# Optimization experiments

Measured on AMD Instinct MI355X. Metric: run time of the kernel, lower is better.

Reference implementation:

```python
import jax, jax.numpy as jnp
import numpy as np

N_NODES = 100000
N_EDGES = 1600000
IN_DIM = 128
OUT_DIM = 64


def setup_inputs() -> dict:
    key = jax.random.key(0)
    k1, k2, k3 = jax.random.split(key, 3)
    x = jax.random.normal(k1, (N_NODES, IN_DIM), dtype=jnp.float32)
    edge_index = jax.random.randint(k2, (2, N_EDGES), 0, N_NODES, dtype=jnp.int64)
    W = jax.random.normal(k3, (IN_DIM, OUT_DIM), dtype=jnp.float32) * (1.0 / np.sqrt(IN_DIM))
    b = jnp.zeros((OUT_DIM,), dtype=jnp.float32)
    return {"x": x, "edge_index": edge_index, "W": W, "b": b}


def reference(x, edge_index, W, b):
    row = edge_index[0]  # source nodes
    col = edge_index[1]  # target nodes (aggregation index)
    n = x.shape[0]

    # gcn_norm with add_self_loops=False: degree from edge weights (ones) at target
    ones = jnp.ones((edge_index.shape[1],), dtype=x.dtype)
    deg = jax.ops.segment_sum(ones, col, num_segments=n)  # [N]
    deg_inv_sqrt = jnp.where(deg > 0, jax.lax.rsqrt(jnp.maximum(deg, 1e-12)), 0.0)
    norm = deg_inv_sqrt[row] * deg_inv_sqrt[col]  # [E]

    # linear transform first (bias added after aggregation, as in PyG GCNConv)
    h = x @ W  # [N, OUT_DIM]

    # gather source features, scale by norm, scatter-add to targets
    msg = h[row] * norm[:, None]  # [E, OUT_DIM]
    out = jax.ops.segment_sum(msg, col, num_segments=n) + b  # [N, OUT_DIM]

    return jax.nn.relu(out)
```

## Files before the change

kernel.cpp:

```cpp
#include <hip/hip_runtime.h>
#include <hip/hip_bf16.h>

#define IN_DIM 128
#define OUT_DIM 64
#define NPB_LOG 9
#define NPB (1 << NPB_LOG)
#define MAXBUCK 1024
#define B1 1024
#define SCAN_TPB 256

static inline size_t align_up(size_t v, size_t a) { return (v + a - 1) & ~(a - 1); }

__device__ __forceinline__ float bf2f(unsigned short u) {
    return __uint_as_float(((unsigned int)u) << 16);
}
__device__ __forceinline__ unsigned short f2bf(float f) {
    unsigned int x = __float_as_uint(f);
    unsigned int r = (x + 0x7fffu + ((x >> 16) & 1u)) >> 16;
    return (unsigned short)r;
}

typedef _Float16 half8 __attribute__((ext_vector_type(8)));
typedef float f32x4 __attribute__((ext_vector_type(4)));

__global__ void __launch_bounds__(256) kA_count(
    const int* __restrict__ col, int* __restrict__ Hist,
    int n_edges, int nbuck, int chunk) {
    __shared__ int hist[MAXBUCK];
    for (int i = threadIdx.x; i < nbuck; i += 256) hist[i] = 0;
    __syncthreads();
    int start = blockIdx.x * chunk;
    int end = min(n_edges, start + chunk);
    for (int i = start + threadIdx.x; i < end; i += 256)
        atomicAdd(&hist[col[i] >> NPB_LOG], 1);
    __syncthreads();
    int* hrow = Hist + (size_t)blockIdx.x * nbuck;
    for (int i = threadIdx.x; i < nbuck; i += 256) hrow[i] = hist[i];
}

__global__ void __launch_bounds__(256) kS1_scanbins(
    const int* __restrict__ Hist, int* __restrict__ Offs,
    int* __restrict__ BinTotal, int nbuck) {
    __shared__ int s[SCAN_TPB];
    int bin = blockIdx.x;
    int t = threadIdx.x;
    int v[4];
#pragma unroll
    for (int j = 0; j < 4; ++j) v[j] = Hist[(size_t)(t * 4 + j) * nbuck + bin];
    int tsum = v[0] + v[1] + v[2] + v[3];
    s[t] = tsum;
    __syncthreads();
    for (int off = 1; off < SCAN_TPB; off <<= 1) {
        int x = (t >= off) ? s[t - off] : 0;
        __syncthreads();
        s[t] += x;
        __syncthreads();
    }
    int run = s[t] - tsum;
#pragma unroll
    for (int j = 0; j < 4; ++j) {
        Offs[(size_t)(t * 4 + j) * nbuck + bin] = run;
        run += v[j];
    }
    if (t == SCAN_TPB - 1) BinTotal[bin] = run;
}

__global__ void __launch_bounds__(256) kS2_scantotals(
    const int* __restrict__ BinTotal, int* __restrict__ BucketStart,
    int* __restrict__ row_start, int nbuck, int n_nodes, int n_edges) {
    __shared__ int s[SCAN_TPB];
    int t = threadIdx.x;
    int v[4];
#pragma unroll
    for (int j = 0; j < 4; ++j) {
        int idx = t * 4 + j;
        v[j] = (idx < nbuck) ? BinTotal[idx] : 0;
    }
    int tsum = v[0] + v[1] + v[2] + v[3];
    s[t] = tsum;
    __syncthreads();
    for (int off = 1; off < SCAN_TPB; off <<= 1) {
        int x = (t >= off) ? s[t - off] : 0;
        __syncthreads();
        s[t] += x;
        __syncthreads();
    }
    int run = s[t] - tsum;
#pragma unroll
    for (int j = 0; j < 4; ++j) {
        int idx = t * 4 + j;
        if (idx < nbuck) BucketStart[idx] = run;
        run += v[j];
    }
    if (t == 0) {
        BucketStart[nbuck] = n_edges;
        row_start[n_nodes] = n_edges;
    }
}

__global__ void __launch_bounds__(256) kB_scatter(
    const int* __restrict__ row, const int* __restrict__ col,
    const int* __restrict__ BucketStart, const int* __restrict__ Offs,
    unsigned int* __restrict__ EdgeBuf, int n_edges, int nbuck, int chunk) {
    __shared__ int cur[MAXBUCK];
    const int* orow = Offs + (size_t)blockIdx.x * nbuck;
    for (int i = threadIdx.x; i < nbuck; i += 256)
        cur[i] = BucketStart[i] + orow[i];
    __syncthreads();
    int start = blockIdx.x * chunk;
    int end = min(n_edges, start + chunk);
    for (int i = start + threadIdx.x; i < end; i += 256) {
        int c = col[i];
        int r = row[i];
        int bin = c >> NPB_LOG;
        int p = atomicAdd(&cur[bin], 1);
        EdgeBuf[p] = ((unsigned int)r << NPB_LOG) | (unsigned int)(c & (NPB - 1));
    }
}

__global__ void __launch_bounds__(256) kC_localsort(
    const unsigned int* __restrict__ EdgeBuf, const int* __restrict__ BucketStart,
    int* __restrict__ row_start, float* __restrict__ dis,
    int* __restrict__ edge_src, int n_nodes) {
    __shared__ int cnt[NPB];
    __shared__ int cur[NPB];
    __shared__ int s[SCAN_TPB];
    int t = threadIdx.x;
    int nb0 = blockIdx.x << NPB_LOG;
    int nn = min(NPB, n_nodes - nb0);
    int es = BucketStart[blockIdx.x];
    int ee = BucketStart[blockIdx.x + 1];

    for (int i = t; i < NPB; i += 256) cnt[i] = 0;
    __syncthreads();
    for (int i = es + t; i < ee; i += 256)
        atomicAdd(&cnt[EdgeBuf[i] & (NPB - 1)], 1);
    __syncthreads();

    int a = cnt[2 * t];
    int b = cnt[2 * t + 1];
    int tsum = a + b;
    s[t] = tsum;
    __syncthreads();
    for (int off = 1; off < SCAN_TPB; off <<= 1) {
        int x = (t >= off) ? s[t - off] : 0;
        __syncthreads();
        s[t] += x;
        __syncthreads();
    }
    int excl = s[t] - tsum;
    if (2 * t < nn) {
        row_start[nb0 + 2 * t] = es + excl;
        dis[nb0 + 2 * t] = (a > 0) ? rsqrtf((float)a) : 0.0f;
    }
    if (2 * t + 1 < nn) {
        row_start[nb0 + 2 * t + 1] = es + excl + a;
        dis[nb0 + 2 * t + 1] = (b > 0) ? rsqrtf((float)b) : 0.0f;
    }
    cur[2 * t] = excl;
    cur[2 * t + 1] = excl + a;
    __syncthreads();

    for (int i = es + t; i < ee; i += 256) {
        unsigned int v = EdgeBuf[i];
        int cl = v & (NPB - 1);
        int r = (int)(v >> NPB_LOG);
        int p = atomicAdd(&cur[cl], 1);
        edge_src[es + p] = r;
    }
}

__global__ void __launch_bounds__(256) k_matmul_mfma(
    const float* __restrict__ x, const float* __restrict__ W,
    const float* __restrict__ dis, unsigned short* __restrict__ h, int n_nodes) {
    const int lane = threadIdx.x & 63;
    const int m = lane & 15;
    const int q = lane >> 4;
    const int wid = (blockIdx.x * blockDim.x + threadIdx.x) >> 6;
    const int ntiles = (n_nodes + 15) >> 4;
    if (wid >= ntiles) return;

    half8 bfrag[4][4];
#pragma unroll
    for (int kt = 0; kt < 4; ++kt) {
#pragma unroll
        for (int nt = 0; nt < 4; ++nt) {
            int k0 = kt * 32 + q * 8;
            int c = nt * 16 + m;
#pragma unroll
            for (int j = 0; j < 8; ++j)
                bfrag[kt][nt][j] = (_Float16)W[(size_t)(k0 + j) * OUT_DIM + c];
        }
    }

    const int nb = wid << 4;
    int arow = nb + m;
    if (arow >= n_nodes) arow = n_nodes - 1;
    const float* xr = x + (size_t)arow * IN_DIM;

    f32x4 acc[4];
#pragma unroll
    for (int nt = 0; nt < 4; ++nt) acc[nt] = (f32x4){0.f, 0.f, 0.f, 0.f};

#pragma unroll
    for (int kt = 0; kt < 4; ++kt) {
        const float4* xp = (const float4*)(xr + kt * 32 + q * 8);
        float4 lo = xp[0];
        float4 hi = xp[1];
        half8 afrag;
        afrag[0] = (_Float16)lo.x; afrag[1] = (_Float16)lo.y;
        afrag[2] = (_Float16)lo.z; afrag[3] = (_Float16)lo.w;
        afrag[4] = (_Float16)hi.x; afrag[5] = (_Float16)hi.y;
        afrag[6] = (_Float16)hi.z; afrag[7] = (_Float16)hi.w;
#pragma unroll
        for (int nt = 0; nt < 4; ++nt)
            acc[nt] = __builtin_amdgcn_mfma_f32_16x16x32_f16(afrag, bfrag[kt][nt],
                                                             acc[nt], 0, 0, 0);
    }

#pragma unroll
    for (int r = 0; r < 4; ++r) {
        int node = nb + q * 4 + r;
        if (node < n_nodes) {
            float dv = dis[node];
            unsigned short* hp = h + (size_t)node * OUT_DIM + m;
#pragma unroll
            for (int nt = 0; nt < 4; ++nt)
                hp[nt * 16] = f2bf(acc[nt][r] * dv);
        }
    }
}

__global__ void __launch_bounds__(256) k_aggregate(
    const int* __restrict__ row_start, const int* __restrict__ edge_src,
    const float* __restrict__ dis, const unsigned short* __restrict__ h,
    const float* __restrict__ b, float* __restrict__ out,
    int n_nodes, int n_edges) {
    const int lane = threadIdx.x & 63;
    int wid = (blockIdx.x * blockDim.x + threadIdx.x) >> 6;
    int nw = (gridDim.x * blockDim.x) >> 6;
    float bias = b[lane];
    for (int c = wid; c < n_nodes; c += nw) {
        int s = row_start[c];
        int e = row_start[c + 1];
        float a0 = 0.0f, a1 = 0.0f, a2 = 0.0f, a3 = 0.0f;
        for (int base = s; base < e; base += 64) {
            int li = base + lane;
            int eidx = edge_src[(li < n_edges) ? li : (n_edges - 1)];
            int cnt = min(64, e - base);
            int j = 0;
            for (; j + 3 < cnt; j += 4) {
                int r0 = __shfl(eidx, j, 64);
                int r1 = __shfl(eidx, j + 1, 64);
                int r2 = __shfl(eidx, j + 2, 64);
                int r3 = __shfl(eidx, j + 3, 64);
                a0 += bf2f(h[(size_t)r0 * OUT_DIM + lane]);
                a1 += bf2f(h[(size_t)r1 * OUT_DIM + lane]);
                a2 += bf2f(h[(size_t)r2 * OUT_DIM + lane]);
                a3 += bf2f(h[(size_t)r3 * OUT_DIM + lane]);
            }
            for (; j < cnt; ++j) {
                int r = __shfl(eidx, j, 64);
                a0 += bf2f(h[(size_t)r * OUT_DIM + lane]);
            }
        }
        float acc = (a0 + a1) + (a2 + a3);
        float v = fmaf(acc, dis[c], bias);
        out[(size_t)c * OUT_DIM + lane] = fmaxf(v, 0.0f);
    }
}

#define MM_NODES 16
__global__ void __launch_bounds__(256) k_matmul_f32(
    const float* __restrict__ x, const float* __restrict__ W,
    const float* __restrict__ dis, float* __restrict__ h, int n_nodes) {
    __shared__ float xs[MM_NODES * IN_DIM];
    const int lane = threadIdx.x & 63;
    const int wv = threadIdx.x >> 6;
    float w[IN_DIM];
#pragma unroll
    for (int k = 0; k < IN_DIM; ++k) w[k] = W[k * OUT_DIM + lane];
    int nchunks = (n_nodes + MM_NODES - 1) / MM_NODES;
    for (int ch = blockIdx.x; ch < nchunks; ch += gridDim.x) {
        int base = ch * MM_NODES;
        int nrows = min(MM_NODES, n_nodes - base);
        __syncthreads();
        const float4* xg = (const float4*)(x + (size_t)base * IN_DIM);
        int nf4 = nrows * IN_DIM / 4;
        for (int i = threadIdx.x; i < nf4; i += 256) ((float4*)xs)[i] = xg[i];
        __syncthreads();
#pragma unroll
        for (int j = 0; j < 4; ++j) {
            int local = wv * 4 + j;
            int node = base + local;
            if (local < nrows) {
                const float4* xr = (const float4*)(xs + local * IN_DIM);
                float acc = 0.0f;
#pragma unroll
                for (int k4 = 0; k4 < IN_DIM / 4; ++k4) {
                    float4 xv = xr[k4];
                    acc = fmaf(xv.x, w[k4 * 4 + 0], acc);
                    acc = fmaf(xv.y, w[k4 * 4 + 1], acc);
                    acc = fmaf(xv.z, w[k4 * 4 + 2], acc);
                    acc = fmaf(xv.w, w[k4 * 4 + 3], acc);
                }
                h[(size_t)node * OUT_DIM + lane] = acc * dis[node];
            }
        }
    }
}

__global__ void k_degree_fb(const int* __restrict__ col, int* __restrict__ deg,
                            int n_edges) {
    int i = blockIdx.x * blockDim.x + threadIdx.x;
    int stride = gridDim.x * blockDim.x;
    for (; i < n_edges; i += stride) atomicAdd(&deg[col[i]], 1);
}

__global__ void k_rsqrt_fb(const int* __restrict__ deg, float* __restrict__ dis, int n) {
    int i = blockIdx.x * blockDim.x + threadIdx.x;
    if (i < n) {
        int d = deg[i];
        dis[i] = (d > 0) ? rsqrtf((float)d) : 0.0f;
    }
}

__global__ void __launch_bounds__(256) k_scatter_fb(
    const int* __restrict__ row, const int* __restrict__ col,
    const float* __restrict__ dis, const float* __restrict__ h,
    float* __restrict__ out, int n_edges) {
    const int lane = threadIdx.x & 63;
    int e = (blockIdx.x * blockDim.x + threadIdx.x) >> 6;
    int nw = (gridDim.x * blockDim.x) >> 6;
    for (; e < n_edges; e += nw) {
        int r = row[e];
        int c = col[e];
        float v = h[(size_t)r * OUT_DIM + lane] * dis[c];
        atomicAdd(&out[(size_t)c * OUT_DIM + lane], v);
    }
}

__global__ void k_bias_relu_fb(float* __restrict__ out, const float* __restrict__ b,
                               int total) {
    int i = blockIdx.x * blockDim.x + threadIdx.x;
    int stride = gridDim.x * blockDim.x;
    for (; i < total; i += stride) {
        float v = out[i] + b[i & (OUT_DIM - 1)];
        out[i] = fmaxf(v, 0.0f);
    }
}

extern "C" void kernel_launch(void* const* d_in, const int* in_sizes, int n_in,
                              void* d_out, int out_size, void* d_ws, size_t ws_size,
                              hipStream_t stream) {
    const float* x = (const float*)d_in[0];
    const int* ei = (const int*)d_in[1];
    const float* W = (const float*)d_in[2];
    const float* b = (const float*)d_in[3];
    float* out = (float*)d_out;

    const int n_nodes = in_sizes[0] / IN_DIM;
    const int n_edges = in_sizes[1] / 2;
    const int* row = ei;
    const int* col = ei + n_edges;

    const int nbuck = (n_nodes + NPB - 1) >> NPB_LOG;
    const int chunk = (n_edges + B1 - 1) / B1;

    char* wsb = (char*)d_ws;
    size_t off = 0;
    int* Hist = (int*)(wsb + off);       off += align_up((size_t)B1 * nbuck * 4, 256);
    int* Offs = (int*)(wsb + off);       off += align_up((size_t)B1 * nbuck * 4, 256);
    int* BinTotal = (int*)(wsb + off);   off += align_up((size_t)nbuck * 4, 256);
    int* BucketStart = (int*)(wsb + off);off += align_up((size_t)(nbuck + 1) * 4, 256);
    int* row_start = (int*)(wsb + off);  off += align_up((size_t)(n_nodes + 1) * 4, 256);
    float* dis = (float*)(wsb + off);    off += align_up((size_t)n_nodes * 4, 256);
    unsigned int* EdgeBuf = (unsigned int*)(wsb + off);
                                         off += align_up((size_t)n_edges * 4, 256);
    int* edge_src = (int*)(wsb + off);   off += align_up((size_t)n_edges * 4, 256);
    unsigned short* h = (unsigned short*)(wsb + off);
                                         off += (size_t)n_nodes * OUT_DIM * 2;
    const size_t needed = off;

    const bool ok = (ws_size >= needed) && (nbuck <= MAXBUCK) &&
                    (n_nodes <= (1 << 23));

    if (ok) {
        kA_count<<<B1, 256, 0, stream>>>(col, Hist, n_edges, nbuck, chunk);
        kS1_scanbins<<<nbuck, 256, 0, stream>>>(Hist, Offs, BinTotal, nbuck);
        kS2_scantotals<<<1, 256, 0, stream>>>(BinTotal, BucketStart, row_start,
                                              nbuck, n_nodes, n_edges);
        kB_scatter<<<B1, 256, 0, stream>>>(row, col, BucketStart, Offs, EdgeBuf,
                                           n_edges, nbuck, chunk);
        kC_localsort<<<nbuck, 256, 0, stream>>>(EdgeBuf, BucketStart, row_start,
                                                dis, edge_src, n_nodes);
        int ntiles = (n_nodes + 15) / 16;
        int mm_blocks = (ntiles + 3) / 4;
        k_matmul_mfma<<<mm_blocks, 256, 0, stream>>>(x, W, dis, h, n_nodes);
        int agg_blocks = (n_nodes + 3) / 4 + 1;
        k_aggregate<<<agg_blocks, 256, 0, stream>>>(row_start, edge_src, dis, h, b,
                                                    out, n_nodes, n_edges);
    } else {
        char* p = (char*)d_ws;
        int* deg_f = (int*)p;
        float* dis_f = (float*)(p + align_up((size_t)n_nodes * 4, 256));
        float* h_f = (float*)(p + 2 * align_up((size_t)n_nodes * 4, 256));
        hipMemsetAsync(deg_f, 0, (size_t)n_nodes * 4, stream);
        hipMemsetAsync(out, 0, (size_t)out_size * 4, stream);
        k_degree_fb<<<1024, 256, 0, stream>>>(col, deg_f, n_edges);
        k_rsqrt_fb<<<(n_nodes + 255) / 256, 256, 0, stream>>>(deg_f, dis_f, n_nodes);
        k_matmul_f32<<<1024, 256, 0, stream>>>(x, W, dis_f, h_f, n_nodes);
        k_scatter_fb<<<2048, 256, 0, stream>>>(row, col, dis_f, h_f, out, n_edges);
        k_bias_relu_fb<<<2048, 256, 0, stream>>>(out, b, n_nodes * OUT_DIM);
    }
}
```

Before: 210.2 us.

## Replace full CSR sort with bucketed LDS-atomic aggregation and atomic bin tickets

Drops the per-node local sort (kC) and the per-bin scan kernel. Bin offsets now come from global atomic tickets, and the bucket size shrinks to 128 nodes. Aggregation runs one block per bucket, accumulating gathered bf16 rows into padded shared-memory float tables with LDS atomics, then applies scale, bias and relu. This removes the second scatter pass and the edge_src buffer, at the cost of many LDS float atomics and 1024-ish large-LDS blocks with a less deterministic summation order.

```diff
diff --git a/kernel.cpp b/kernel.cpp
--- a/kernel.cpp
+++ b/kernel.cpp
@@ -3,11 +3,11 @@
 
 #define IN_DIM 128
 #define OUT_DIM 64
-#define NPB_LOG 9
+#define NPB_LOG 7
 #define NPB (1 << NPB_LOG)
 #define MAXBUCK 1024
-#define B1 1024
-#define SCAN_TPB 256
+#define B1 512
+#define ACC_STRIDE 65
 
 static inline size_t align_up(size_t v, size_t a) { return (v + a - 1) & ~(a - 1); }
 
@@ -23,34 +23,40 @@
 typedef _Float16 half8 __attribute__((ext_vector_type(8)));
 typedef float f32x4 __attribute__((ext_vector_type(4)));
 
-__global__ void __launch_bounds__(256) kA_count(
-    const int* __restrict__ col, int* __restrict__ Hist,
-    int n_edges, int nbuck, int chunk) {
+__global__ void __launch_bounds__(256) kA_ticket(
+    const int* __restrict__ col, int* __restrict__ BinTotal,
+    int* __restrict__ tickets, int n_edges, int nbuck, int chunk) {
     __shared__ int hist[MAXBUCK];
-    for (int i = threadIdx.x; i < nbuck; i += 256) hist[i] = 0;
+    int t = threadIdx.x;
+    for (int i = t; i < nbuck; i += 256) hist[i] = 0;
     __syncthreads();
     int start = blockIdx.x * chunk;
     int end = min(n_edges, start + chunk);
-    for (int i = start + threadIdx.x; i < end; i += 256)
+    for (int i = start + t; i < end; i += 256)
         atomicAdd(&hist[col[i] >> NPB_LOG], 1);
     __syncthreads();
-    int* hrow = Hist + (size_t)blockIdx.x * nbuck;
-    for (int i = threadIdx.x; i < nbuck; i += 256) hrow[i] = hist[i];
-}
-
-__global__ void __launch_bounds__(256) kS1_scanbins(
-    const int* __restrict__ Hist, int* __restrict__ Offs,
-    int* __restrict__ BinTotal, int nbuck) {
-    __shared__ int s[SCAN_TPB];
-    int bin = blockIdx.x;
+    int* trow = tickets + (size_t)blockIdx.x * nbuck;
+    for (int i = t; i < nbuck; i += 256) {
+        int cv = hist[i];
+        trow[i] = atomicAdd(&BinTotal[i], cv);
+    }
+}
+
+__global__ void __launch_bounds__(256) kS2_scantotals(
+    const int* __restrict__ BinTotal, int* __restrict__ BucketStart,
+    int nbuck, int n_edges) {
+    __shared__ int s[256];
     int t = threadIdx.x;
     int v[4];
 #pragma unroll
-    for (int j = 0; j < 4; ++j) v[j] = Hist[(size_t)(t * 4 + j) * nbuck + bin];
+    for (int j = 0; j < 4; ++j) {
+        int idx = t * 4 + j;
+        v[j] = (idx < nbuck) ? BinTotal[idx] : 0;
+    }
     int tsum = v[0] + v[1] + v[2] + v[3];
     s[t] = tsum;
     __syncthreads();
-    for (int off = 1; off < SCAN_TPB; off <<= 1) {
+    for (int off = 1; off < 256; off <<= 1) {
         int x = (t >= off) ? s[t - off] : 0;
         __syncthreads();
         s[t] += x;
@@ -59,57 +65,26 @@
     int run = s[t] - tsum;
 #pragma unroll
     for (int j = 0; j < 4; ++j) {
-        Offs[(size_t)(t * 4 + j) * nbuck + bin] = run;
-        run += v[j];
-    }
-    if (t == SCAN_TPB - 1) BinTotal[bin] = run;
-}
-
-__global__ void __launch_bounds__(256) kS2_scantotals(
-    const int* __restrict__ BinTotal, int* __restrict__ BucketStart,
-    int* __restrict__ row_start, int nbuck, int n_nodes, int n_edges) {
-    __shared__ int s[SCAN_TPB];
-    int t = threadIdx.x;
-    int v[4];
-#pragma unroll
-    for (int j = 0; j < 4; ++j) {
-        int idx = t * 4 + j;
-        v[j] = (idx < nbuck) ? BinTotal[idx] : 0;
-    }
-    int tsum = v[0] + v[1] + v[2] + v[3];
-    s[t] = tsum;
-    __syncthreads();
-    for (int off = 1; off < SCAN_TPB; off <<= 1) {
-        int x = (t >= off) ? s[t - off] : 0;
-        __syncthreads();
-        s[t] += x;
-        __syncthreads();
-    }
-    int run = s[t] - tsum;
-#pragma unroll
-    for (int j = 0; j < 4; ++j) {
         int idx = t * 4 + j;
         if (idx < nbuck) BucketStart[idx] = run;
         run += v[j];
     }
-    if (t == 0) {
-        BucketStart[nbuck] = n_edges;
-        row_start[n_nodes] = n_edges;
-    }
+    if (t == 0) BucketStart[nbuck] = n_edges;
 }
 
 __global__ void __launch_bounds__(256) kB_scatter(
     const int* __restrict__ row, const int* __restrict__ col,
-    const int* __restrict__ BucketStart, const int* __restrict__ Offs,
+    const int* __restrict__ BucketStart, const int* __restrict__ tickets,
     unsigned int* __restrict__ EdgeBuf, int n_edges, int nbuck, int chunk) {
     __shared__ int cur[MAXBUCK];
-    const int* orow = Offs + (size_t)blockIdx.x * nbuck;
-    for (int i = threadIdx.x; i < nbuck; i += 256)
-        cur[i] = BucketStart[i] + orow[i];
+    const int* trow = tickets + (size_t)blockIdx.x * nbuck;
+    int t = threadIdx.x;
+    for (int i = t; i < nbuck; i += 256)
+        cur[i] = BucketStart[i] + trow[i];
     __syncthreads();
     int start = blockIdx.x * chunk;
     int end = min(n_edges, start + chunk);
-    for (int i = start + threadIdx.x; i < end; i += 256) {
+    for (int i = start + t; i < end; i += 256) {
         int c = col[i];
         int r = row[i];
         int bin = c >> NPB_LOG;
@@ -118,55 +93,25 @@
     }
 }
 
-__global__ void __launch_bounds__(256) kC_localsort(
+__global__ void __launch_bounds__(256) kD_degree(
     const unsigned int* __restrict__ EdgeBuf, const int* __restrict__ BucketStart,
-    int* __restrict__ row_start, float* __restrict__ dis,
-    int* __restrict__ edge_src, int n_nodes) {
+    float* __restrict__ dis, int n_nodes) {
     __shared__ int cnt[NPB];
-    __shared__ int cur[NPB];
-    __shared__ int s[SCAN_TPB];
-    int t = threadIdx.x;
-    int nb0 = blockIdx.x << NPB_LOG;
-    int nn = min(NPB, n_nodes - nb0);
+    int t = threadIdx.x;
+    if (t < NPB) cnt[t] = 0;
+    __syncthreads();
     int es = BucketStart[blockIdx.x];
     int ee = BucketStart[blockIdx.x + 1];
-
-    for (int i = t; i < NPB; i += 256) cnt[i] = 0;
-    __syncthreads();
     for (int i = es + t; i < ee; i += 256)
         atomicAdd(&cnt[EdgeBuf[i] & (NPB - 1)], 1);
     __syncthreads();
-
-    int a = cnt[2 * t];
-    int b = cnt[2 * t + 1];
-    int tsum = a + b;
-    s[t] = tsum;
-    __syncthreads();
-    for (int off = 1; off < SCAN_TPB; off <<= 1) {
-        int x = (t >= off) ? s[t - off] : 0;
-        __syncthreads();
-        s[t] += x;
-        __syncthreads();
-    }
-    int excl = s[t] - tsum;
-    if (2 * t < nn) {
-        row_start[nb0 + 2 * t] = es + excl;
-        dis[nb0 + 2 * t] = (a > 0) ? rsqrtf((float)a) : 0.0f;
-    }
-    if (2 * t + 1 < nn) {
-        row_start[nb0 + 2 * t + 1] = es + excl + a;
-        dis[nb0 + 2 * t + 1] = (b > 0) ? rsqrtf((float)b) : 0.0f;
-    }
-    cur[2 * t] = excl;
-    cur[2 * t + 1] = excl + a;
-    __syncthreads();
-
-    for (int i = es + t; i < ee; i += 256) {
-        unsigned int v = EdgeBuf[i];
-        int cl = v & (NPB - 1);
-        int r = (int)(v >> NPB_LOG);
-        int p = atomicAdd(&cur[cl], 1);
-        edge_src[es + p] = r;
+    int nb0 = blockIdx.x << NPB_LOG;
+    if (t < NPB) {
+        int node = nb0 + t;
+        if (node < n_nodes) {
+            int d = cnt[t];
+            dis[node] = (d > 0) ? rsqrtf((float)d) : 0.0f;
+        }
     }
 }
 
@@ -231,42 +176,61 @@
     }
 }
 
-__global__ void __launch_bounds__(256) k_aggregate(
-    const int* __restrict__ row_start, const int* __restrict__ edge_src,
+__global__ void __launch_bounds__(512) kE_aggregate(
+    const unsigned int* __restrict__ EdgeBuf, const int* __restrict__ BucketStart,
     const float* __restrict__ dis, const unsigned short* __restrict__ h,
-    const float* __restrict__ b, float* __restrict__ out,
-    int n_nodes, int n_edges) {
-    const int lane = threadIdx.x & 63;
-    int wid = (blockIdx.x * blockDim.x + threadIdx.x) >> 6;
-    int nw = (gridDim.x * blockDim.x) >> 6;
-    float bias = b[lane];
-    for (int c = wid; c < n_nodes; c += nw) {
-        int s = row_start[c];
-        int e = row_start[c + 1];
-        float a0 = 0.0f, a1 = 0.0f, a2 = 0.0f, a3 = 0.0f;
-        for (int base = s; base < e; base += 64) {
-            int li = base + lane;
-            int eidx = edge_src[(li < n_edges) ? li : (n_edges - 1)];
-            int cnt = min(64, e - base);
-            int j = 0;
-            for (; j + 3 < cnt; j += 4) {
-                int r0 = __shfl(eidx, j, 64);
-                int r1 = __shfl(eidx, j + 1, 64);
-                int r2 = __shfl(eidx, j + 2, 64);
-                int r3 = __shfl(eidx, j + 3, 64);
-                a0 += bf2f(h[(size_t)r0 * OUT_DIM + lane]);
-                a1 += bf2f(h[(size_t)r1 * OUT_DIM + lane]);
-                a2 += bf2f(h[(size_t)r2 * OUT_DIM + lane]);
-                a3 += bf2f(h[(size_t)r3 * OUT_DIM + lane]);
-            }
-            for (; j < cnt; ++j) {
-                int r = __shfl(eidx, j, 64);
-                a0 += bf2f(h[(size_t)r * OUT_DIM + lane]);
-            }
-        }
-        float acc = (a0 + a1) + (a2 + a3);
-        float v = fmaf(acc, dis[c], bias);
-        out[(size_t)c * OUT_DIM + lane] = fmaxf(v, 0.0f);
+    const float* __restrict__ b, float* __restrict__ out, int n_nodes) {
+    __shared__ float accL[NPB * ACC_STRIDE];
+    int t = threadIdx.x;
+    for (int i = t; i < NPB * ACC_STRIDE; i += 512) accL[i] = 0.0f;
+    int es = BucketStart[blockIdx.x];
+    int ee = BucketStart[blockIdx.x + 1];
+    int nb0 = blockIdx.x << NPB_LOG;
+    int nn = min(NPB, n_nodes - nb0);
+    __syncthreads();
+
+    const int lane = t & 63;
+    const int wv = t >> 6;
+    const int quarter = lane >> 4;
+    const int qlane = lane & 15;
+
+    for (int base = es + wv * 8; base < ee; base += 64) {
+        int iA = base + quarter;
+        int iB = base + quarter + 4;
+        unsigned int eA = EdgeBuf[iA < ee ? iA : es];
+        unsigned int eB = EdgeBuf[iB < ee ? iB : es];
+        int rA = (int)(eA >> NPB_LOG), cA = (int)(eA & (NPB - 1));
+        int rB = (int)(eB >> NPB_LOG), cB = (int)(eB & (NPB - 1));
+        uint2 vA = make_uint2(0u, 0u), vB = make_uint2(0u, 0u);
+        if (iA < ee) vA = *(const uint2*)(h + (size_t)rA * OUT_DIM + qlane * 4);
+        if (iB < ee) vB = *(const uint2*)(h + (size_t)rB * OUT_DIM + qlane * 4);
+        if (iA < ee) {
+            float* ap = accL + cA * ACC_STRIDE + qlane * 4;
+            atomicAdd(ap + 0, __uint_as_float(vA.x << 16));
+            atomicAdd(ap + 1, __uint_as_float(vA.x & 0xFFFF0000u));
+            atomicAdd(ap + 2, __uint_as_float(vA.y << 16));
+            atomicAdd(ap + 3, __uint_as_float(vA.y & 0xFFFF0000u));
+        }
+        if (iB < ee) {
+            float* bp = accL + cB * ACC_STRIDE + qlane * 4;
+            atomicAdd(bp + 0, __uint_as_float(vB.x << 16));
+            atomicAdd(bp + 1, __uint_as_float(vB.x & 0xFFFF0000u));
+            atomicAdd(bp + 2, __uint_as_float(vB.y << 16));
+            atomicAdd(bp + 3, __uint_as_float(vB.y & 0xFFFF0000u));
+        }
+    }
+    __syncthreads();
+
+    int q4 = (t & 15) * 4;
+    for (int nl = (t >> 4); nl < nn; nl += 32) {
+        float dv = dis[nb0 + nl];
+        const float* ap = accL + nl * ACC_STRIDE + q4;
+        float4 o;
+        o.x = fmaxf(fmaf(ap[0], dv, b[q4 + 0]), 0.0f);
+        o.y = fmaxf(fmaf(ap[1], dv, b[q4 + 1]), 0.0f);
+        o.z = fmaxf(fmaf(ap[2], dv, b[q4 + 2]), 0.0f);
+        o.w = fmaxf(fmaf(ap[3], dv, b[q4 + 3]), 0.0f);
+        *(float4*)(out + (size_t)(nb0 + nl) * OUT_DIM + q4) = o;
     }
 }
 
@@ -369,37 +333,32 @@
 
     char* wsb = (char*)d_ws;
     size_t off = 0;
-    int* Hist = (int*)(wsb + off);       off += align_up((size_t)B1 * nbuck * 4, 256);
-    int* Offs = (int*)(wsb + off);       off += align_up((size_t)B1 * nbuck * 4, 256);
     int* BinTotal = (int*)(wsb + off);   off += align_up((size_t)nbuck * 4, 256);
     int* BucketStart = (int*)(wsb + off);off += align_up((size_t)(nbuck + 1) * 4, 256);
-    int* row_start = (int*)(wsb + off);  off += align_up((size_t)(n_nodes + 1) * 4, 256);
+    int* tickets = (int*)(wsb + off);    off += align_up((size_t)B1 * nbuck * 4, 256);
     float* dis = (float*)(wsb + off);    off += align_up((size_t)n_nodes * 4, 256);
     unsigned int* EdgeBuf = (unsigned int*)(wsb + off);
                                          off += align_up((size_t)n_edges * 4, 256);
-    int* edge_src = (int*)(wsb + off);   off += align_up((size_t)n_edges * 4, 256);
     unsigned short* h = (unsigned short*)(wsb + off);
                                          off += (size_t)n_nodes * OUT_DIM * 2;
     const size_t needed = off;
 
     const bool ok = (ws_size >= needed) && (nbuck <= MAXBUCK) &&
-                    (n_nodes <= (1 << 23));
+                    (n_nodes <= (NPB * MAXBUCK)) && (n_nodes <= (1 << 23));
 
     if (ok) {
-        kA_count<<<B1, 256, 0, stream>>>(col, Hist, n_edges, nbuck, chunk);
-        kS1_scanbins<<<nbuck, 256, 0, stream>>>(Hist, Offs, BinTotal, nbuck);
-        kS2_scantotals<<<1, 256, 0, stream>>>(BinTotal, BucketStart, row_start,
-                                              nbuck, n_nodes, n_edges);
-        kB_scatter<<<B1, 256, 0, stream>>>(row, col, BucketStart, Offs, EdgeBuf,
+        hipMemsetAsync(BinTotal, 0, (size_t)nbuck * 4, stream);
+        kA_ticket<<<B1, 256, 0, stream>>>(col, BinTotal, tickets, n_edges, nbuck,
+                                          chunk);
+        kS2_scantotals<<<1, 256, 0, stream>>>(BinTotal, BucketStart, nbuck, n_edges);
+        kB_scatter<<<B1, 256, 0, stream>>>(row, col, BucketStart, tickets, EdgeBuf,
                                            n_edges, nbuck, chunk);
-        kC_localsort<<<nbuck, 256, 0, stream>>>(EdgeBuf, BucketStart, row_start,
-                                                dis, edge_src, n_nodes);
+        kD_degree<<<nbuck, 256, 0, stream>>>(EdgeBuf, BucketStart, dis, n_nodes);
         int ntiles = (n_nodes + 15) / 16;
         int mm_blocks = (ntiles + 3) / 4;
         k_matmul_mfma<<<mm_blocks, 256, 0, stream>>>(x, W, dis, h, n_nodes);
-        int agg_blocks = (n_nodes + 3) / 4 + 1;
-        k_aggregate<<<agg_blocks, 256, 0, stream>>>(row_start, edge_src, dis, h, b,
-                                                    out, n_nodes, n_edges);
+        kE_aggregate<<<nbuck, 512, 0, stream>>>(EdgeBuf, BucketStart, dis, h, b,
+                                                out, n_nodes);
     } else {
         char* p = (char*)d_ws;
         int* deg_f = (int*)p;
```

New measurement: 828.0 us. 3.94x slower.
